# Kernel tuning notes

Measured on AMD Instinct MI355X. Metric: run time of the kernel, lower is better.

## Reference

```python
import jax, jax.numpy as jnp
import numpy as np

N = 100000      # nodes
E = 1280000     # edges
D_IN = 64       # in_channels
D_OUT = 64      # out_channels
D_EDGE = 16     # edge_dim
NEG_SLOPE = 0.01  # torch F.leaky_relu default


def setup_inputs() -> dict:
    key = jax.random.key(0)
    ks = jax.random.split(key, 8)
    x = jax.random.normal(ks[0], (N, D_IN), dtype=jnp.float32)
    edge_attr = jax.random.normal(ks[1], (E, D_EDGE), dtype=jnp.float32)
    src = jax.random.randint(ks[2], (E,), 0, N, dtype=jnp.int32)
    dst = jax.random.randint(ks[3], (E,), 0, N, dtype=jnp.int32)
    # parameters (xavier-like scale)
    W1 = jax.random.normal(ks[4], (D_OUT, D_IN + D_EDGE), dtype=jnp.float32) * (2.0 / (D_OUT + D_IN + D_EDGE)) ** 0.5
    W2 = jax.random.normal(ks[5], (D_OUT, D_IN), dtype=jnp.float32) * (2.0 / (D_OUT + D_IN)) ** 0.5
    attn = jax.random.normal(ks[6], (D_OUT + D_IN,), dtype=jnp.float32) * (2.0 / (1 + D_OUT + D_IN)) ** 0.5
    bias = jnp.zeros((D_OUT,), dtype=jnp.float32)
    return {"x": x, "edge_attr": edge_attr, "src": src, "dst": dst,
            "W1": W1, "W2": W2, "attn": attn, "bias": bias}


def reference(x, edge_attr, src, dst, W1, W2, attn, bias):
    # node transform: lin2
    x_t = x @ W2.T                                    # [N, D_OUT]
    # per-edge gathers
    x_l = x[src]                                      # [E, D_IN]
    x_r = x[dst]                                      # [E, D_IN]
    # lin1 on [x_l || edge_attr]
    f_srt = jnp.concatenate([x_l, edge_attr], axis=-1) @ W1.T   # [E, D_OUT]
    e = jax.nn.leaky_relu(jnp.concatenate([f_srt, x_r], axis=-1), NEG_SLOPE)  # [E, D_OUT+D_IN]
    logits = e @ attn                                 # [E]
    # edge_softmax over destination-node segments
    seg_max = jax.ops.segment_max(logits, dst, num_segments=N)
    seg_max = jnp.where(jnp.isfinite(seg_max), seg_max, 0.0)
    expd = jnp.exp(logits - seg_max[dst])             # [E]
    denom = jax.ops.segment_sum(expd, dst, num_segments=N)
    alpha = expd / denom[dst]                         # [E]  (dropout p=0 -> identity)
    # scatter-sum aggregation: sum_e alpha_e * x_t[src_e] into dst
    msgs = x_t[src] * alpha[:, None]                  # [E, D_OUT]
    h = jax.ops.segment_sum(msgs, dst, num_segments=N)
    return h + bias
```

## Files before the change

### kernel.cpp

```cpp
#include <hip/hip_runtime.h>

#define D 64
#define D_EDGE 16
#define NEG 0.01f

typedef unsigned int  uint32;
typedef unsigned short ushort16;

__device__ __forceinline__ float leaky(float v) { return fmaxf(v, NEG * v); }

__device__ __forceinline__ ushort16 f2bf(float f) {
    uint32 b = __float_as_uint(f);
    uint32 r = b + 0x7fffu + ((b >> 16) & 1u);
    return (ushort16)(r >> 16);
}
__device__ __forceinline__ float bf2f(ushort16 u) {
    return __uint_as_float(((uint32)u) << 16);
}
__device__ __forceinline__ float bf_lo(uint32 w) { return __uint_as_float(w << 16); }
__device__ __forceinline__ float bf_hi(uint32 w) { return __uint_as_float(w & 0xffff0000u); }

__global__ __launch_bounds__(256) void node_kernel(
    const float* __restrict__ x, const float* __restrict__ W1,
    const float* __restrict__ W2,
    ushort16* __restrict__ Abf, ushort16* __restrict__ xtb, int N_)
{
    __shared__ float w2s[64 * 64];
    __shared__ float w1s[64 * 64];
    for (int i = threadIdx.x; i < 64 * 64; i += 256) {
        w2s[i] = W2[i];
        int k = i >> 6, j = i & 63;
        w1s[i] = W1[k * 80 + j];
    }
    __syncthreads();

    const int lane = threadIdx.x & 63;
    const int q    = threadIdx.x >> 6;
    const int n    = blockIdx.x * 64 + lane;
    if (n >= N_) return;

    const float4* x4 = (const float4*)(x + (size_t)n * D);
    float4 xr[16];
#pragma unroll
    for (int i = 0; i < 16; i++) xr[i] = x4[i];

    const float4* w2s4 = (const float4*)w2s;
    const float4* w1s4 = (const float4*)w1s;

    uint32* Au = (uint32*)Abf;
    uint32* Xu = (uint32*)xtb;

    float a_prev = 0.f, b_prev = 0.f;
#pragma unroll
    for (int kk = 0; kk < 16; kk++) {
        const int k = q * 16 + kk;
        float a = 0.f, b = 0.f;
#pragma unroll
        for (int j = 0; j < 16; j++) {
            float4 w = w2s4[k * 16 + j];
            a += xr[j].x * w.x + xr[j].y * w.y + xr[j].z * w.z + xr[j].w * w.w;
            float4 u = w1s4[k * 16 + j];
            b += xr[j].x * u.x + xr[j].y * u.y + xr[j].z * u.z + xr[j].w * u.w;
        }
        if (kk & 1) {
            Xu[(size_t)n * 32 + (k >> 1)] = (uint32)f2bf(a_prev) | ((uint32)f2bf(a) << 16);
            Au[(size_t)n * 32 + (k >> 1)] = (uint32)f2bf(b_prev) | ((uint32)f2bf(b) << 16);
        } else {
            a_prev = a; b_prev = b;
        }
    }
}

__global__ __launch_bounds__(256) void hist_kernel(
    const int* __restrict__ dst, int* __restrict__ cnt, int E_)
{
    int i = blockIdx.x * 256 + threadIdx.x;
    if (i < E_) atomicAdd(cnt + dst[i], 1);
}

__global__ __launch_bounds__(256) void scan1(
    const int* __restrict__ cnt, int* __restrict__ part, int N_)
{
    __shared__ int sm[256];
    const int b = blockIdx.x, t = threadIdx.x;
    const int i0 = b * 1024 + t * 4;
    int s = 0;
    if (i0     < N_) s += cnt[i0];
    if (i0 + 1 < N_) s += cnt[i0 + 1];
    if (i0 + 2 < N_) s += cnt[i0 + 2];
    if (i0 + 3 < N_) s += cnt[i0 + 3];
    sm[t] = s; __syncthreads();
    for (int off = 128; off > 0; off >>= 1) {
        if (t < off) sm[t] += sm[t + off];
        __syncthreads();
    }
    if (t == 0) part[b] = sm[0];
}

__global__ __launch_bounds__(256) void scan2(int* __restrict__ part, int nb)
{
    __shared__ int sm[256];
    const int t = threadIdx.x;
    int v = (t < nb) ? part[t] : 0;
    sm[t] = v; __syncthreads();
    for (int off = 1; off < 256; off <<= 1) {
        int a = (t >= off) ? sm[t - off] : 0;
        __syncthreads();
        sm[t] += a;
        __syncthreads();
    }
    if (t < nb) part[t] = sm[t] - v;
}

__global__ __launch_bounds__(256) void scan3(
    const int* __restrict__ cnt, const int* __restrict__ part,
    int* __restrict__ rowst, int N_)
{
    __shared__ int sm[256];
    const int b = blockIdx.x, t = threadIdx.x;
    const int i0 = b * 1024 + t * 4;
    int c0 = 0, c1 = 0, c2 = 0, c3 = 0;
    if (i0     < N_) c0 = cnt[i0];
    if (i0 + 1 < N_) c1 = cnt[i0 + 1];
    if (i0 + 2 < N_) c2 = cnt[i0 + 2];
    if (i0 + 3 < N_) c3 = cnt[i0 + 3];
    const int s = c0 + c1 + c2 + c3;
    sm[t] = s; __syncthreads();
    for (int off = 1; off < 256; off <<= 1) {
        int a = (t >= off) ? sm[t - off] : 0;
        __syncthreads();
        sm[t] += a;
        __syncthreads();
    }
    const int base = part[b] + (sm[t] - s);
    if (i0     < N_) rowst[i0]     = base;
    if (i0 + 1 < N_) rowst[i0 + 1] = base + c0;
    if (i0 + 2 < N_) rowst[i0 + 2] = base + c0 + c1;
    if (i0 + 3 < N_) rowst[i0 + 3] = base + c0 + c1 + c2;
}

__global__ __launch_bounds__(256) void edge_kernel(
    const float* __restrict__ edge_attr, const int* __restrict__ src,
    const int* __restrict__ dst, const float* __restrict__ W1,
    const float* __restrict__ attn, const ushort16* __restrict__ Abf,
    int* __restrict__ rowpos, int2* __restrict__ SP, int E_)
{
    const int e = blockIdx.x * 256 + threadIdx.x;
    if (e >= E_) return;

    const int s = src[e];
    const int d = dst[e];

    uint32 Ad[32];
    {
        const uint4* Ap = (const uint4*)(Abf + (size_t)s * D);
#pragma unroll
        for (int i = 0; i < 8; i++) *(uint4*)(Ad + 4 * i) = Ap[i];
    }
    float Ef[16];
    {
        const float4* Ep = (const float4*)(edge_attr + (size_t)e * D_EDGE);
#pragma unroll
        for (int i = 0; i < 4; i++) *(float4*)(Ef + 4 * i) = Ep[i];
    }

    float v = 0.f;
#pragma unroll
    for (int j = 0; j < 32; ++j) {
        const float4* w0 = (const float4*)(W1 + (2 * j) * 80 + 64);
        const float4* w1 = (const float4*)(W1 + (2 * j + 1) * 80 + 64);
        float4 p0 = w0[0], p1 = w0[1], p2 = w0[2], p3 = w0[3];
        float4 q0 = w1[0], q1 = w1[1], q2 = w1[2], q3 = w1[3];

        float g0 = bf_lo(Ad[j]);
        float g1 = bf_hi(Ad[j]);

        g0 = fmaf(Ef[ 0], p0.x, g0); g1 = fmaf(Ef[ 0], q0.x, g1);
        g0 = fmaf(Ef[ 1], p0.y, g0); g1 = fmaf(Ef[ 1], q0.y, g1);
        g0 = fmaf(Ef[ 2], p0.z, g0); g1 = fmaf(Ef[ 2], q0.z, g1);
        g0 = fmaf(Ef[ 3], p0.w, g0); g1 = fmaf(Ef[ 3], q0.w, g1);
        g0 = fmaf(Ef[ 4], p1.x, g0); g1 = fmaf(Ef[ 4], q1.x, g1);
        g0 = fmaf(Ef[ 5], p1.y, g0); g1 = fmaf(Ef[ 5], q1.y, g1);
        g0 = fmaf(Ef[ 6], p1.z, g0); g1 = fmaf(Ef[ 6], q1.z, g1);
        g0 = fmaf(Ef[ 7], p1.w, g0); g1 = fmaf(Ef[ 7], q1.w, g1);
        g0 = fmaf(Ef[ 8], p2.x, g0); g1 = fmaf(Ef[ 8], q2.x, g1);
        g0 = fmaf(Ef[ 9], p2.y, g0); g1 = fmaf(Ef[ 9], q2.y, g1);
        g0 = fmaf(Ef[10], p2.z, g0); g1 = fmaf(Ef[10], q2.z, g1);
        g0 = fmaf(Ef[11], p2.w, g0); g1 = fmaf(Ef[11], q2.w, g1);
        g0 = fmaf(Ef[12], p3.x, g0); g1 = fmaf(Ef[12], q3.x, g1);
        g0 = fmaf(Ef[13], p3.y, g0); g1 = fmaf(Ef[13], q3.y, g1);
        g0 = fmaf(Ef[14], p3.z, g0); g1 = fmaf(Ef[14], q3.z, g1);
        g0 = fmaf(Ef[15], p3.w, g0); g1 = fmaf(Ef[15], q3.w, g1);

        v = fmaf(leaky(g0), attn[2 * j],     v);
        v = fmaf(leaky(g1), attn[2 * j + 1], v);
    }

    const float p = __expf(v);
    const int pos = atomicAdd(rowpos + d, 1);
    SP[pos] = make_int2(s, __float_as_int(p));
}

__global__ __launch_bounds__(256) void agg_kernel(
    const ushort16* __restrict__ xtb, const int2* __restrict__ SP,
    const int* __restrict__ rowend, const float* __restrict__ bias,
    float* __restrict__ out, int N_)
{
    const int n    = blockIdx.x * 4 + (threadIdx.x >> 6);
    const int lane = threadIdx.x & 63;
    if (n >= N_) return;

    const int end   = rowend[n];
    const int start = n ? rowend[n - 1] : 0;

    float acc = 0.f, den = 0.f;
    int i = start;
    for (; i + 3 < end; i += 4) {
        int2 a = SP[i], b = SP[i + 1], c = SP[i + 2], d = SP[i + 3];
        float pa = __int_as_float(a.y), pb = __int_as_float(b.y);
        float pc = __int_as_float(c.y), pd = __int_as_float(d.y);
        float ma = bf2f(xtb[(size_t)a.x * D + lane]);
        float mb = bf2f(xtb[(size_t)b.x * D + lane]);
        float mc = bf2f(xtb[(size_t)c.x * D + lane]);
        float md = bf2f(xtb[(size_t)d.x * D + lane]);
        acc = fmaf(pa, ma, fmaf(pb, mb, fmaf(pc, mc, fmaf(pd, md, acc))));
        den += (pa + pb) + (pc + pd);
    }
    for (; i < end; i++) {
        int2 a = SP[i];
        float pa = __int_as_float(a.y);
        acc = fmaf(pa, bf2f(xtb[(size_t)a.x * D + lane]), acc);
        den += pa;
    }

    float sc = den > 0.f ? 1.f / den : 0.f;
    out[(size_t)n * D + lane] = fmaf(acc, sc, bias[lane]);
}

extern "C" void kernel_launch(void* const* d_in, const int* in_sizes, int n_in,
                              void* d_out, int out_size, void* d_ws, size_t ws_size,
                              hipStream_t stream)
{
    const float* x         = (const float*)d_in[0];
    const float* edge_attr = (const float*)d_in[1];
    const int*   src       = (const int*)d_in[2];
    const int*   dst       = (const int*)d_in[3];
    const float* W1        = (const float*)d_in[4];
    const float* W2        = (const float*)d_in[5];
    const float* attn      = (const float*)d_in[6];
    const float* bias      = (const float*)d_in[7];
    float* out = (float*)d_out;

    const int N_ = in_sizes[0] / D;
    const int E_ = in_sizes[2];

    char* w = (char*)d_ws;
    ushort16* Abf  = (ushort16*)w;  w += (size_t)N_ * D * sizeof(ushort16);
    ushort16* xtb  = (ushort16*)w;  w += (size_t)N_ * D * sizeof(ushort16);
    int2*     SP   = (int2*)w;      w += (size_t)E_ * sizeof(int2);
    int*      rowst= (int*)w;       w += (size_t)N_ * sizeof(int);
    int*      cnt  = (int*)w;       w += (size_t)N_ * sizeof(int);
    int*      part = (int*)w;

    hipMemsetAsync(cnt, 0, (size_t)N_ * sizeof(int), stream);

    const int NB1 = (N_ + 1023) / 1024;

    hist_kernel<<<(E_ + 255) / 256, 256, 0, stream>>>(dst, cnt, E_);
    scan1<<<NB1, 256, 0, stream>>>(cnt, part, N_);
    scan2<<<1, 256, 0, stream>>>(part, NB1);
    scan3<<<NB1, 256, 0, stream>>>(cnt, part, rowst, N_);

    node_kernel<<<(N_ + 63) / 64, 256, 0, stream>>>(x, W1, W2, Abf, xtb, N_);

    edge_kernel<<<(E_ + 255) / 256, 256, 0, stream>>>(edge_attr, src, dst, W1,
                                                      attn, Abf, rowst, SP, E_);

    agg_kernel<<<(N_ + 3) / 4, 256, 0, stream>>>(xtb, SP, rowst, bias, out, N_);
}
```

Measured before the change: 409.8 us.

## Stage node outputs through LDS for coalesced stores; split agg wave into halves

The node kernel now loads each block's x rows cooperatively into shared memory, reads weights straight from global/cache instead of staging them in LDS, and writes the bf16 results back through LDS as 16-byte coalesced stores rather than strided 4-byte stores per node. The aggregation kernel has each half-wave process alternate edges with 32-bit packed bf16 loads (two channels per lane), then combines the halves with a cross-lane shuffle. The aim is to cut uncoalesced global traffic and get more gathers in flight per edge. The cost is extra LDS traffic and syncs in the node kernel, and an idle half-wave in the tail loop of the aggregation kernel.

```diff
diff --git a/kernel.cpp b/kernel.cpp
--- a/kernel.cpp
+++ b/kernel.cpp
@@ -25,48 +25,65 @@
     const float* __restrict__ W2,
     ushort16* __restrict__ Abf, ushort16* __restrict__ xtb, int N_)
 {
-    __shared__ float w2s[64 * 64];
-    __shared__ float w1s[64 * 64];
-    for (int i = threadIdx.x; i < 64 * 64; i += 256) {
-        w2s[i] = W2[i];
-        int k = i >> 6, j = i & 63;
-        w1s[i] = W1[k * 80 + j];
+    __shared__ float xs[64][68];
+    uint32* sA = (uint32*)&xs[0][0];
+    uint32* sX = sA + 64 * 33;
+
+    const int tid = threadIdx.x;
+    const int b0  = blockIdx.x * 64;
+
+    for (int idx = tid; idx < 64 * 16; idx += 256) {
+        const int rr = idx >> 4, cc = idx & 15;
+        float4 v = make_float4(0.f, 0.f, 0.f, 0.f);
+        if (b0 + rr < N_) v = ((const float4*)(x + (size_t)(b0 + rr) * D))[cc];
+        *(float4*)&xs[rr][cc * 4] = v;
     }
     __syncthreads();
 
-    const int lane = threadIdx.x & 63;
-    const int q    = threadIdx.x >> 6;
-    const int n    = blockIdx.x * 64 + lane;
-    if (n >= N_) return;
-
-    const float4* x4 = (const float4*)(x + (size_t)n * D);
+    const int lane = tid & 63;
+    const int q    = __builtin_amdgcn_readfirstlane(tid >> 6);
+
     float4 xr[16];
 #pragma unroll
-    for (int i = 0; i < 16; i++) xr[i] = x4[i];
-
-    const float4* w2s4 = (const float4*)w2s;
-    const float4* w1s4 = (const float4*)w1s;
-
-    uint32* Au = (uint32*)Abf;
-    uint32* Xu = (uint32*)xtb;
+    for (int i = 0; i < 16; i++) xr[i] = *(const float4*)&xs[lane][4 * i];
+    __syncthreads();
 
     float a_prev = 0.f, b_prev = 0.f;
 #pragma unroll
     for (int kk = 0; kk < 16; kk++) {
         const int k = q * 16 + kk;
+        const float4* w2r = (const float4*)(W2 + (size_t)k * 64);
+        const float4* w1r = (const float4*)(W1 + (size_t)k * 80);
         float a = 0.f, b = 0.f;
 #pragma unroll
         for (int j = 0; j < 16; j++) {
-            float4 w = w2s4[k * 16 + j];
+            float4 w = w2r[j];
             a += xr[j].x * w.x + xr[j].y * w.y + xr[j].z * w.z + xr[j].w * w.w;
-            float4 u = w1s4[k * 16 + j];
+            float4 u = w1r[j];
             b += xr[j].x * u.x + xr[j].y * u.y + xr[j].z * u.z + xr[j].w * u.w;
         }
         if (kk & 1) {
-            Xu[(size_t)n * 32 + (k >> 1)] = (uint32)f2bf(a_prev) | ((uint32)f2bf(a) << 16);
-            Au[(size_t)n * 32 + (k >> 1)] = (uint32)f2bf(b_prev) | ((uint32)f2bf(b) << 16);
+            const int pr = k >> 1;
+            sX[lane * 33 + pr] = (uint32)f2bf(a_prev) | ((uint32)f2bf(a) << 16);
+            sA[lane * 33 + pr] = (uint32)f2bf(b_prev) | ((uint32)f2bf(b) << 16);
         } else {
             a_prev = a; b_prev = b;
+        }
+    }
+    __syncthreads();
+
+    uint32* Au = (uint32*)Abf;
+    uint32* Xu = (uint32*)xtb;
+    const size_t gbase = (size_t)b0 * 32;
+    for (int base = tid * 4; base < 2048; base += 1024) {
+        const int nn = base >> 5, cc = base & 31;
+        if (b0 + nn < N_) {
+            const uint32* ra = sA + nn * 33 + cc;
+            const uint32* rx = sX + nn * 33 + cc;
+            uint4 va = make_uint4(ra[0], ra[1], ra[2], ra[3]);
+            uint4 vx = make_uint4(rx[0], rx[1], rx[2], rx[3]);
+            *(uint4*)(Au + gbase + base) = va;
+            *(uint4*)(Xu + gbase + base) = vx;
         }
     }
 }
@@ -209,32 +226,54 @@
     const int n    = blockIdx.x * 4 + (threadIdx.x >> 6);
     const int lane = threadIdx.x & 63;
     if (n >= N_) return;
+    const int half = lane >> 5;
+    const int c    = lane & 31;
 
     const int end   = rowend[n];
     const int start = n ? rowend[n - 1] : 0;
-
-    float acc = 0.f, den = 0.f;
+    const uint32* X = (const uint32*)xtb;
+
+    float accx = 0.f, accy = 0.f, den = 0.f;
     int i = start;
-    for (; i + 3 < end; i += 4) {
-        int2 a = SP[i], b = SP[i + 1], c = SP[i + 2], d = SP[i + 3];
-        float pa = __int_as_float(a.y), pb = __int_as_float(b.y);
-        float pc = __int_as_float(c.y), pd = __int_as_float(d.y);
-        float ma = bf2f(xtb[(size_t)a.x * D + lane]);
-        float mb = bf2f(xtb[(size_t)b.x * D + lane]);
-        float mc = bf2f(xtb[(size_t)c.x * D + lane]);
-        float md = bf2f(xtb[(size_t)d.x * D + lane]);
-        acc = fmaf(pa, ma, fmaf(pb, mb, fmaf(pc, mc, fmaf(pd, md, acc))));
-        den += (pa + pb) + (pc + pd);
+    for (; i + 7 < end; i += 8) {
+        int2 A0 = SP[i+0], A1 = SP[i+1], A2 = SP[i+2], A3 = SP[i+3];
+        int2 A4 = SP[i+4], A5 = SP[i+5], A6 = SP[i+6], A7 = SP[i+7];
+        int   r0 = half ? A1.x : A0.x;  float p0 = __int_as_float(half ? A1.y : A0.y);
+        int   r1 = half ? A3.x : A2.x;  float p1 = __int_as_float(half ? A3.y : A2.y);
+        int   r2 = half ? A5.x : A4.x;  float p2 = __int_as_float(half ? A5.y : A4.y);
+        int   r3 = half ? A7.x : A6.x;  float p3 = __int_as_float(half ? A7.y : A6.y);
+        uint32 u0 = X[(size_t)r0 * 32 + c];
+        uint32 u1 = X[(size_t)r1 * 32 + c];
+        uint32 u2 = X[(size_t)r2 * 32 + c];
+        uint32 u3 = X[(size_t)r3 * 32 + c];
+        accx = fmaf(p0, bf_lo(u0), accx); accy = fmaf(p0, bf_hi(u0), accy);
+        accx = fmaf(p1, bf_lo(u1), accx); accy = fmaf(p1, bf_hi(u1), accy);
+        accx = fmaf(p2, bf_lo(u2), accx); accy = fmaf(p2, bf_hi(u2), accy);
+        accx = fmaf(p3, bf_lo(u3), accx); accy = fmaf(p3, bf_hi(u3), accy);
+        den += (p0 + p1) + (p2 + p3);
     }
     for (; i < end; i++) {
         int2 a = SP[i];
-        float pa = __int_as_float(a.y);
-        acc = fmaf(pa, bf2f(xtb[(size_t)a.x * D + lane]), acc);
-        den += pa;
-    }
-
-    float sc = den > 0.f ? 1.f / den : 0.f;
-    out[(size_t)n * D + lane] = fmaf(acc, sc, bias[lane]);
+        if (half == 0) {
+            float p = __int_as_float(a.y);
+            uint32 u = X[(size_t)a.x * 32 + c];
+            accx = fmaf(p, bf_lo(u), accx);
+            accy = fmaf(p, bf_hi(u), accy);
+            den += p;
+        }
+    }
+    accx += __shfl_xor(accx, 32, 64);
+    accy += __shfl_xor(accy, 32, 64);
+    den  += __shfl_xor(den,  32, 64);
+
+    if (half == 0) {
+        const float sc = den > 0.f ? 1.f / den : 0.f;
+        const float2 bb = *(const float2*)(bias + 2 * c);
+        float2 o;
+        o.x = fmaf(accx, sc, bb.x);
+        o.y = fmaf(accy, sc, bb.y);
+        *(float2*)(out + (size_t)n * D + 2 * c) = o;
+    }
 }
 
 extern "C" void kernel_launch(void* const* d_in, const int* in_sizes, int n_in,
```

New measurement: 414.2 us. About the same (+1.1%).
